# Kernel tuning notes

Hardware: AMD Instinct MI355X
Metric: run time of the kernel (lower is better)

Reference implementation:

```python
import jax, jax.numpy as jnp
import numpy as np


def setup_inputs() -> dict:
    key = jax.random.key(0)
    k1, _ = jax.random.split(key)
    B, S, D = 4, 4096, 64
    inp = jax.random.normal(k1, (B, S, D), dtype=jnp.float32)
    attn_mask = jnp.zeros((S, S), dtype=bool)  # no masked positions
    return {"input": inp, "attn_mask": attn_mask}


def reference(input, attn_mask):
    # attn_mask: bool [S,S] -> additive mask with -inf at masked positions
    am = jnp.where(attn_mask, -jnp.inf, 0.0).T  # transpose(0,1)
    # scores: [B,S,S]
    v = jnp.einsum('bsd,btd->bst', input, input)
    mask = (1.0 - am) * -10000.0
    v = v + mask  # dead in original module too: w is drawn fresh below
    # w = empty_like(v).uniform_(-0.1, 0.1)
    wkey = jax.random.key(42)
    w = jax.random.uniform(wkey, v.shape, dtype=v.dtype, minval=-0.1, maxval=0.1)
    w = jax.nn.softmax(w, axis=-1)
    # per-column (dim 1) L1 renorm: w[:, i] /= ||w[:, i]||_1 over (batch, last dim)
    denom = jnp.sum(jnp.abs(w), axis=(0, 2), keepdims=True)  # [1,S,1]
    w = w / denom
    return jnp.einsum('bst,btd->bsd', w, input)
```

## Files before the change

kernel.cpp:

```cpp
#include <hip/hip_runtime.h>
#include <hip/hip_bf16.h>
#include <stdint.h>


#define S_ 4096
#define D_ 64

#define EXP_A32 ((float)(0.2 * 1.4426950408889634 / 4294967296.0))
#define EXP_B   ((float)(-0.1 * 1.4426950408889634))

typedef __attribute__((ext_vector_type(8))) short short8v;
typedef __attribute__((ext_vector_type(4))) float floatx4;

__device__ __forceinline__ void tf8(uint32_t c0, uint32_t r[8]) {
    const uint32_t k1 = 42u, k2 = 0x1BD11BDAu ^ 42u;
    uint32_t a[8], b[8];
#pragma unroll
    for (int i = 0; i < 8; ++i) { a[i] = 0u; b[i] = c0 + (uint32_t)i + k1; }
#define TF_RND(rot)                                          \
    _Pragma("unroll")                                        \
    for (int i = 0; i < 8; ++i) {                            \
        a[i] += b[i];                                        \
        b[i] = __builtin_rotateleft32(b[i], (rot));          \
        b[i] ^= a[i];                                        \
    }
#define TF_INJ(ka, kb)                                       \
    _Pragma("unroll")                                        \
    for (int i = 0; i < 8; ++i) { a[i] += (ka); b[i] += (kb); }
    TF_RND(13) TF_RND(15) TF_RND(26) TF_RND(6)
    TF_INJ(k1, k2 + 1u)
    TF_RND(17) TF_RND(29) TF_RND(16) TF_RND(24)
    TF_INJ(k2, 2u)
    TF_RND(13) TF_RND(15) TF_RND(26) TF_RND(6)
    TF_INJ(0u, k1 + 3u)
    TF_RND(17) TF_RND(29) TF_RND(16) TF_RND(24)
    TF_INJ(k1, k2 + 4u)
    TF_RND(13) TF_RND(15) TF_RND(26) TF_RND(6)
    TF_INJ(k2, 5u)
#undef TF_RND
#undef TF_INJ
#pragma unroll
    for (int i = 0; i < 8; ++i) r[i] = a[i] ^ b[i];
}

__device__ __forceinline__ uint32_t cvt_pk_bf16(float e0, float e1) {
    uint32_t r;
    asm("v_cvt_pk_bf16_f32 %0, %1, %2" : "=v"(r) : "v"(e0), "v"(e1));
    return r;
}

__device__ __forceinline__ short8v gen_a(uint32_t c0) {
    uint32_t r[8];
    tf8(c0, r);
    float e[8];
#pragma unroll
    for (int i = 0; i < 8; ++i) {
        const float fm = (float)r[i];
        e[i] = __builtin_amdgcn_exp2f(__builtin_fmaf(fm, EXP_A32, EXP_B));
    }
    union { uint32_t u[4]; short8v v; } a;
#pragma unroll
    for (int i = 0; i < 4; ++i) a.u[i] = cvt_pk_bf16(e[2 * i], e[2 * i + 1]);
    return a.v;
}

__global__ __launch_bounds__(64) void pack_xt_bf16(
    const float* __restrict__ x, short* __restrict__ bf)
{
    const int id = blockIdx.x;
    const int l  = threadIdx.x;
    const int dg = id & 3;
    const int kc = (id >> 2) & 1;
    const int kt = (id >> 3) & 63;
    const int b  = id >> 9;
    const int d  = dg * 16 + (l & 15);
    const int k0 = kt * 64 + kc * 32 + (l >> 4) * 8;
    const float* __restrict__ xb = x + (size_t)b * (S_ * D_);
    union { short8v v; short s[8]; } r;
#pragma unroll
    for (int j = 0; j < 8; ++j) {
        __hip_bfloat16 h = __float2bfloat16(xb[(size_t)(k0 + j) * D_ + d]);
        r.s[j] = __builtin_bit_cast(short, h);
    }
    *(short8v*)&bf[(size_t)id * 512 + l * 8] = r.v;
}

__global__ __launch_bounds__(512, 4) void fused_rand_attn_mfma5(
    const short* __restrict__ bf, float* __restrict__ out)
{
    const int tid  = threadIdx.x;
    const int bid  = (blockIdx.x & 7) * 128 + (blockIdx.x >> 3);
    const int b    = bid >> 8;
    const int s0   = (bid & 255) * 16;
    const int w    = tid >> 6;
    const int lane = tid & 63;
    const int lt   = lane & 15;
    const int lh   = lane >> 4;

    __shared__ float ACC[8][4][64][4];
    __shared__ float ZL[8][16];

    floatx4 acc0 = {0.f,0.f,0.f,0.f}, acc1 = {0.f,0.f,0.f,0.f};
    floatx4 acc2 = {0.f,0.f,0.f,0.f}, acc3 = {0.f,0.f,0.f,0.f};
    floatx4 accz = {0.f,0.f,0.f,0.f};

    const short one_bf = (short)0x3F80;
    const short8v bones = {one_bf, one_bf, one_bf, one_bf,
                           one_bf, one_bf, one_bf, one_bf};

    const short* __restrict__ bl =
        bf + (size_t)b * (64 * 4096) + (size_t)lane * 8;
    const uint32_t fl = (((uint32_t)b << 24) | ((uint32_t)(s0 + lt) << 12))
                        + (uint32_t)(lh * 8);

#pragma unroll 1
    for (int kt = w; kt < 64; kt += 8) {
        const short* pk = bl + (size_t)kt * 4096;
        const uint32_t kb = fl + ((uint32_t)kt << 6);

        const short8v b00 = *(const short8v*)(pk);
        const short8v b10 = *(const short8v*)(pk + 512);
        const short8v b20 = *(const short8v*)(pk + 1024);
        const short8v b30 = *(const short8v*)(pk + 1536);
        const short8v b01 = *(const short8v*)(pk + 2048);
        const short8v b11 = *(const short8v*)(pk + 2560);
        const short8v b21 = *(const short8v*)(pk + 3072);
        const short8v b31 = *(const short8v*)(pk + 3584);

        const short8v a0 = gen_a(kb);
        const short8v a1 = gen_a(kb + 32u);

        acc0 = __builtin_amdgcn_mfma_f32_16x16x32_bf16(a0, b00, acc0, 0, 0, 0);
        acc1 = __builtin_amdgcn_mfma_f32_16x16x32_bf16(a0, b10, acc1, 0, 0, 0);
        acc2 = __builtin_amdgcn_mfma_f32_16x16x32_bf16(a0, b20, acc2, 0, 0, 0);
        acc3 = __builtin_amdgcn_mfma_f32_16x16x32_bf16(a0, b30, acc3, 0, 0, 0);
        accz = __builtin_amdgcn_mfma_f32_16x16x32_bf16(a0, bones, accz, 0, 0, 0);
        acc0 = __builtin_amdgcn_mfma_f32_16x16x32_bf16(a1, b01, acc0, 0, 0, 0);
        acc1 = __builtin_amdgcn_mfma_f32_16x16x32_bf16(a1, b11, acc1, 0, 0, 0);
        acc2 = __builtin_amdgcn_mfma_f32_16x16x32_bf16(a1, b21, acc2, 0, 0, 0);
        acc3 = __builtin_amdgcn_mfma_f32_16x16x32_bf16(a1, b31, acc3, 0, 0, 0);
        accz = __builtin_amdgcn_mfma_f32_16x16x32_bf16(a1, bones, accz, 0, 0, 0);
    }

    if (lt == 0) {
#pragma unroll
        for (int r = 0; r < 4; ++r) ZL[w][lh * 4 + r] = accz[r];
    }
    *(floatx4*)&ACC[w][0][lane][0] = acc0;
    *(floatx4*)&ACC[w][1][lane][0] = acc1;
    *(floatx4*)&ACC[w][2][lane][0] = acc2;
    *(floatx4*)&ACC[w][3][lane][0] = acc3;
    __syncthreads();

    const int dg = w & 3;
    const int rh = w >> 2;
    floatx4 facc = {0.f,0.f,0.f,0.f};
#pragma unroll
    for (int w2 = 0; w2 < 8; ++w2) {
        const floatx4 t = *(const floatx4*)&ACC[w2][dg][lane][0];
        facc.x += t.x; facc.y += t.y; facc.z += t.z; facc.w += t.w;
    }
    const float v0 = rh ? facc.z : facc.x;
    const float v1 = rh ? facc.w : facc.y;
    const int row0 = lh * 4 + rh * 2;
    float Z0 = 0.f, Z1 = 0.f;
#pragma unroll
    for (int w2 = 0; w2 < 8; ++w2) {
        Z0 += ZL[w2][row0];
        Z1 += ZL[w2][row0 + 1];
    }
    const int col = dg * 16 + lt;
    out[((size_t)b * S_ + (s0 + row0)) * D_ + col]     = v0 * (0.25f / Z0);
    out[((size_t)b * S_ + (s0 + row0 + 1)) * D_ + col] = v1 * (0.25f / Z1);
}

extern "C" void kernel_launch(void* const* d_in, const int* in_sizes, int n_in,
                              void* d_out, int out_size, void* d_ws, size_t ws_size,
                              hipStream_t stream) {
    const float* x = (const float*)d_in[0];
    float* out = (float*)d_out;
    short* bfw = (short*)d_ws;
    (void)in_sizes; (void)n_in; (void)out_size; (void)ws_size;
    hipLaunchKernelGGL(pack_xt_bf16, dim3(2048), dim3(64), 0, stream, x, bfw);
    hipLaunchKernelGGL(fused_rand_attn_mfma5, dim3(1024), dim3(512), 0, stream,
                       bfw, out);
}
```

Measured before the change: 133.9 us.

## Split waves into producer RNG generators and consumer MFMA waves via LDS ring

Restructures the fused kernel so four waves generate the random softmax weights (Threefry plus exp) into a shared-memory ring buffer. The other four waves consume them with MFMA against the packed bf16 input, one wave per 16-column output group. The row normaliser is now summed in fp32 by the producers instead of an extra MFMA against a ones vector, and the cross-wave accumulator reduction is removed. It adds a block-wide barrier every iteration, serialises each consumer's MFMA chain, and raises the launch-bounds occupancy hint. The RNG work now runs on half the waves, which may make the producers the bottleneck.

New measurement: 135.0 us. About the same (+0.8%).

```diff
diff --git a/kernel.cpp b/kernel.cpp
--- a/kernel.cpp
+++ b/kernel.cpp
@@ -49,7 +49,7 @@
     return r;
 }
 
-__device__ __forceinline__ short8v gen_a(uint32_t c0) {
+__device__ __forceinline__ short8v gen_a(uint32_t c0, float& zp0, float& zp1) {
     uint32_t r[8];
     tf8(c0, r);
     float e[8];
@@ -58,6 +58,8 @@
         const float fm = (float)r[i];
         e[i] = __builtin_amdgcn_exp2f(__builtin_fmaf(fm, EXP_A32, EXP_B));
     }
+    zp0 += (e[0] + e[2]) + (e[4] + e[6]);
+    zp1 += (e[1] + e[3]) + (e[5] + e[7]);
     union { uint32_t u[4]; short8v v; } a;
 #pragma unroll
     for (int i = 0; i < 4; ++i) a.u[i] = cvt_pk_bf16(e[2 * i], e[2 * i + 1]);
@@ -85,7 +87,7 @@
     *(short8v*)&bf[(size_t)id * 512 + l * 8] = r.v;
 }
 
-__global__ __launch_bounds__(512, 4) void fused_rand_attn_mfma5(
+__global__ __launch_bounds__(512, 8) void fused_rand_attn_pc(
     const short* __restrict__ bf, float* __restrict__ out)
 {
     const int tid  = threadIdx.x;
@@ -97,81 +99,73 @@
     const int lt   = lane & 15;
     const int lh   = lane >> 4;
 
-    __shared__ float ACC[8][4][64][4];
-    __shared__ float ZL[8][16];
+    __shared__ short Wring[8][2][512];
+    __shared__ float ZL[4][16];
 
-    floatx4 acc0 = {0.f,0.f,0.f,0.f}, acc1 = {0.f,0.f,0.f,0.f};
-    floatx4 acc2 = {0.f,0.f,0.f,0.f}, acc3 = {0.f,0.f,0.f,0.f};
-    floatx4 accz = {0.f,0.f,0.f,0.f};
-
-    const short one_bf = (short)0x3F80;
-    const short8v bones = {one_bf, one_bf, one_bf, one_bf,
-                           one_bf, one_bf, one_bf, one_bf};
-
+    float zp0 = 0.f, zp1 = 0.f;
+    const uint32_t fbase = ((uint32_t)b << 24) | ((uint32_t)(s0 + lt) << 12)
+                           | (uint32_t)(lh * 8);
+    floatx4 acc = {0.f, 0.f, 0.f, 0.f};
+    const int dgc = (w >= 4) ? (w - 4) : 0;
     const short* __restrict__ bl =
-        bf + (size_t)b * (64 * 4096) + (size_t)lane * 8;
-    const uint32_t fl = (((uint32_t)b << 24) | ((uint32_t)(s0 + lt) << 12))
-                        + (uint32_t)(lh * 8);
+        bf + (size_t)b * 262144 + dgc * 512 + (size_t)lane * 8;
 
 #pragma unroll 1
-    for (int kt = w; kt < 64; kt += 8) {
-        const short* pk = bl + (size_t)kt * 4096;
-        const uint32_t kb = fl + ((uint32_t)kt << 6);
-
-        const short8v b00 = *(const short8v*)(pk);
-        const short8v b10 = *(const short8v*)(pk + 512);
-        const short8v b20 = *(const short8v*)(pk + 1024);
-        const short8v b30 = *(const short8v*)(pk + 1536);
-        const short8v b01 = *(const short8v*)(pk + 2048);
-        const short8v b11 = *(const short8v*)(pk + 2560);
-        const short8v b21 = *(const short8v*)(pk + 3072);
-        const short8v b31 = *(const short8v*)(pk + 3584);
-
-        const short8v a0 = gen_a(kb);
-        const short8v a1 = gen_a(kb + 32u);
-
-        acc0 = __builtin_amdgcn_mfma_f32_16x16x32_bf16(a0, b00, acc0, 0, 0, 0);
-        acc1 = __builtin_amdgcn_mfma_f32_16x16x32_bf16(a0, b10, acc1, 0, 0, 0);
-        acc2 = __builtin_amdgcn_mfma_f32_16x16x32_bf16(a0, b20, acc2, 0, 0, 0);
-        acc3 = __builtin_amdgcn_mfma_f32_16x16x32_bf16(a0, b30, acc3, 0, 0, 0);
-        accz = __builtin_amdgcn_mfma_f32_16x16x32_bf16(a0, bones, accz, 0, 0, 0);
-        acc0 = __builtin_amdgcn_mfma_f32_16x16x32_bf16(a1, b01, acc0, 0, 0, 0);
-        acc1 = __builtin_amdgcn_mfma_f32_16x16x32_bf16(a1, b11, acc1, 0, 0, 0);
-        acc2 = __builtin_amdgcn_mfma_f32_16x16x32_bf16(a1, b21, acc2, 0, 0, 0);
-        acc3 = __builtin_amdgcn_mfma_f32_16x16x32_bf16(a1, b31, acc3, 0, 0, 0);
-        accz = __builtin_amdgcn_mfma_f32_16x16x32_bf16(a1, bones, accz, 0, 0, 0);
+    for (int j = 0; j < 16; ++j) {
+        if (w < 4) {
+            const int kt = 4 * j + w;
+            const int sl = kt & 7;
+            const uint32_t kb = fbase + ((uint32_t)kt << 6);
+            const short8v a0 = gen_a(kb, zp0, zp1);
+            const short8v a1 = gen_a(kb + 32u, zp0, zp1);
+            *(short8v*)&Wring[sl][0][lane * 8] = a0;
+            *(short8v*)&Wring[sl][1][lane * 8] = a1;
+        } else if (j > 0) {
+            const int kt0 = 4 * (j - 1);
+#pragma unroll
+            for (int q = 0; q < 4; ++q) {
+                const int kt = kt0 + q;
+                const short* pb = bl + (size_t)kt * 4096;
+                const short8v A0 = *(const short8v*)&Wring[kt & 7][0][lane * 8];
+                const short8v B0 = *(const short8v*)(pb);
+                acc = __builtin_amdgcn_mfma_f32_16x16x32_bf16(A0, B0, acc, 0,0,0);
+                const short8v A1 = *(const short8v*)&Wring[kt & 7][1][lane * 8];
+                const short8v B1 = *(const short8v*)(pb + 2048);
+                acc = __builtin_amdgcn_mfma_f32_16x16x32_bf16(A1, B1, acc, 0,0,0);
+            }
+        }
+        __syncthreads();
     }
 
-    if (lt == 0) {
+    if (w >= 4) {
 #pragma unroll
-        for (int r = 0; r < 4; ++r) ZL[w][lh * 4 + r] = accz[r];
+        for (int q = 0; q < 4; ++q) {
+            const int kt = 60 + q;
+            const short* pb = bl + (size_t)kt * 4096;
+            const short8v A0 = *(const short8v*)&Wring[kt & 7][0][lane * 8];
+            const short8v B0 = *(const short8v*)(pb);
+            acc = __builtin_amdgcn_mfma_f32_16x16x32_bf16(A0, B0, acc, 0,0,0);
+            const short8v A1 = *(const short8v*)&Wring[kt & 7][1][lane * 8];
+            const short8v B1 = *(const short8v*)(pb + 2048);
+            acc = __builtin_amdgcn_mfma_f32_16x16x32_bf16(A1, B1, acc, 0,0,0);
+        }
+    } else {
+        float zp = zp0 + zp1;
+        zp += __shfl_xor(zp, 16);
+        zp += __shfl_xor(zp, 32);
+        if (lane < 16) ZL[w][lane] = zp;
     }
-    *(floatx4*)&ACC[w][0][lane][0] = acc0;
-    *(floatx4*)&ACC[w][1][lane][0] = acc1;
-    *(floatx4*)&ACC[w][2][lane][0] = acc2;
-    *(floatx4*)&ACC[w][3][lane][0] = acc3;
     __syncthreads();
 
-    const int dg = w & 3;
-    const int rh = w >> 2;
-    floatx4 facc = {0.f,0.f,0.f,0.f};
+    if (w >= 4) {
+        const int col = dgc * 16 + lt;
 #pragma unroll
-    for (int w2 = 0; w2 < 8; ++w2) {
-        const floatx4 t = *(const floatx4*)&ACC[w2][dg][lane][0];
-        facc.x += t.x; facc.y += t.y; facc.z += t.z; facc.w += t.w;
+        for (int r = 0; r < 4; ++r) {
+            const int row = lh * 4 + r;
+            const float Z = (ZL[0][row] + ZL[1][row]) + (ZL[2][row] + ZL[3][row]);
+            out[((size_t)b * S_ + (s0 + row)) * D_ + col] = acc[r] * (0.25f / Z);
+        }
     }
-    const float v0 = rh ? facc.z : facc.x;
-    const float v1 = rh ? facc.w : facc.y;
-    const int row0 = lh * 4 + rh * 2;
-    float Z0 = 0.f, Z1 = 0.f;
-#pragma unroll
-    for (int w2 = 0; w2 < 8; ++w2) {
-        Z0 += ZL[w2][row0];
-        Z1 += ZL[w2][row0 + 1];
-    }
-    const int col = dg * 16 + lt;
-    out[((size_t)b * S_ + (s0 + row0)) * D_ + col]     = v0 * (0.25f / Z0);
-    out[((size_t)b * S_ + (s0 + row0 + 1)) * D_ + col] = v1 * (0.25f / Z1);
 }
 
 extern "C" void kernel_launch(void* const* d_in, const int* in_sizes, int n_in,
@@ -182,6 +176,6 @@
     short* bfw = (short*)d_ws;
     (void)in_sizes; (void)n_in; (void)out_size; (void)ws_size;
     hipLaunchKernelGGL(pack_xt_bf16, dim3(2048), dim3(64), 0, stream, x, bfw);
-    hipLaunchKernelGGL(fused_rand_attn_mfma5, dim3(1024), dim3(512), 0, stream,
+    hipLaunchKernelGGL(fused_rand_attn_pc, dim3(1024), dim3(512), 0, stream,
                        bfw, out);
 }
```
